# Kernel tuning notes

Hardware: AMD Instinct MI355X
Metric: run time of the kernel (lower is better)

The kernel has to match this reference:

```python
import jax, jax.numpy as jnp
import numpy as np

N = 100000      # nodes
E = 3200000     # edges (avg degree 32)
FEA = 67
HID = 16
OUT = 2
K = 3           # num_stacks
T = 2           # num_layers


def setup_inputs() -> dict:
    key = jax.random.key(0)
    ks = jax.random.split(key, 11)
    s = 0.1  # weight init scale
    return {
        "x": jax.random.normal(ks[0], (N, FEA), jnp.float32),
        "edge_index": jax.random.randint(ks[1], (2, E), 0, N, dtype=jnp.int32),
        "init_w1": jax.random.normal(ks[2], (K, FEA, HID), jnp.float32) * s,
        "w1": jax.random.normal(ks[3], (1, K, HID, HID), jnp.float32) * s,
        "root_w1": jax.random.normal(ks[4], (1, K, FEA, HID), jnp.float32) * s,
        "b1": jax.random.normal(ks[5], (1, K, 1, HID), jnp.float32) * s,
        "init_w2": jax.random.normal(ks[6], (K, HID, OUT), jnp.float32) * s,
        "w2": jax.random.normal(ks[7], (1, K, OUT, OUT), jnp.float32) * s,
        "root_w2": jax.random.normal(ks[8], (1, K, HID, OUT), jnp.float32) * s,
        "b2": jax.random.normal(ks[9], (1, K, 1, OUT), jnp.float32) * s,
    }


def gcn_norm(src, dst, n):
    # symmetric normalization of A WITHOUT self-loops (PyG ARMAConv behavior)
    deg = jax.ops.segment_sum(jnp.ones(src.shape[0], jnp.float32), dst, num_segments=n)
    dinv = jnp.where(deg > 0, jax.lax.rsqrt(jnp.maximum(deg, 1.0)), 0.0)
    return dinv[src] * dinv[dst]  # [E]


def arma_conv(x, src, dst, norm, init_w, w, root_w, bias, act, n):
    # x: [N, Fin]; shared_weights=True, num_layers=T, num_stacks=K
    out = jnp.einsum('nf,kfh->knh', x, init_w)           # t=0 transform
    root = jnp.einsum('nf,kfh->knh', x, root_w[0])       # root term (dropout=identity in eval)
    for t in range(T):
        if t > 0:
            out = jnp.einsum('knh,khp->knp', out, w[0])
        # propagate: out[i] = sum_{(j->i)} norm_e * out[j]
        m = (out[:, src, :] * norm[None, :, None]).transpose(1, 0, 2)  # [E,K,H]
        agg = jax.ops.segment_sum(m, dst, num_segments=n).transpose(1, 0, 2)  # [K,N,H]
        out = agg + root + bias[0]
        if act:
            out = jax.nn.relu(out)
    return out.mean(axis=0)  # average over stacks -> [N, H]


def reference(x, edge_index, init_w1, w1, root_w1, b1, init_w2, w2, root_w2, b2):
    src, dst = edge_index[0], edge_index[1]
    n = x.shape[0]
    norm = gcn_norm(src, dst, n)
    h = jax.nn.relu(arma_conv(x, src, dst, norm, init_w1, w1, root_w1, b1, True, n))
    o = arma_conv(h, src, dst, norm, init_w2, w2, root_w2, b2, False, n)
    return jax.nn.log_softmax(o, axis=1)
```

## Files before the change

kernel.cpp:

```cpp
#include <hip/hip_runtime.h>
#include <hip/hip_fp16.h>
#include <math.h>

#define NN 100000
#define NE 3200000
#define FEA 67
#define HID 16
#define OUTC 2
#define KS 3
#define KH 48
#define KO 6
#define PAD 64

#define PB 512
#define EPB 6250
#define BINW 512
#define NBINS 196
#define M1 (NBINS * PB)
#define NSCB 98

#define TBM 128
#define TNB ((NN + TBM - 1) / TBM)
#define XS_STRIDE 132
#define WT_STRIDE 68


__global__ void k_hist(const int* __restrict__ dst, int* __restrict__ hist) {
    __shared__ int h[NBINS];
    if (threadIdx.x < NBINS) h[threadIdx.x] = 0;
    __syncthreads();
    int base = blockIdx.x * EPB;
    for (int i = threadIdx.x; i < EPB; i += 256)
        atomicAdd(&h[dst[base + i] >> 9], 1);
    __syncthreads();
    if (threadIdx.x < NBINS) hist[threadIdx.x * PB + blockIdx.x] = h[threadIdx.x];
}


__global__ void k_partial(const int* __restrict__ in, int* __restrict__ partials, int n) {
    __shared__ int s[256];
    int base = blockIdx.x * 1024;
    int acc = 0;
    for (int i = threadIdx.x; i < 1024; i += 256) {
        int idx = base + i;
        if (idx < n) acc += in[idx];
    }
    s[threadIdx.x] = acc;
    __syncthreads();
    for (int off = 128; off > 0; off >>= 1) {
        if (threadIdx.x < off) s[threadIdx.x] += s[threadIdx.x + off];
        __syncthreads();
    }
    if (threadIdx.x == 0) partials[blockIdx.x] = s[0];
}

__global__ void k_downsweepF(const int* __restrict__ in, const int* __restrict__ partials,
                             int* __restrict__ out, int n) {
    __shared__ int ps[256];
    __shared__ int s[256];
    int t = threadIdx.x;
    ps[t] = (t < NSCB) ? partials[t] : 0;
    __syncthreads();
    for (int off = 1; off < 256; off <<= 1) {
        int v = (t >= off) ? ps[t - off] : 0;
        __syncthreads();
        ps[t] += v;
        __syncthreads();
    }
    int bbase = (blockIdx.x > 0) ? ps[blockIdx.x - 1] : 0;

    int base = blockIdx.x * 1024 + t * 4;
    int d0 = 0, d1 = 0, d2 = 0, d3 = 0;
    if (base + 0 < n) d0 = in[base + 0];
    if (base + 1 < n) d1 = in[base + 1];
    if (base + 2 < n) d2 = in[base + 2];
    if (base + 3 < n) d3 = in[base + 3];
    int ts = d0 + d1 + d2 + d3;
    s[t] = ts;
    __syncthreads();
    for (int off = 1; off < 256; off <<= 1) {
        int v = (t >= off) ? s[t - off] : 0;
        __syncthreads();
        s[t] += v;
        __syncthreads();
    }
    int excl = s[t] - ts + bbase;
    if (base + 0 < n) out[base + 0] = excl;
    if (base + 1 < n) out[base + 1] = excl + d0;
    if (base + 2 < n) out[base + 2] = excl + d0 + d1;
    if (base + 3 < n) out[base + 3] = excl + d0 + d1 + d2;
}


__global__ void k_pass2(const int* __restrict__ src, const int* __restrict__ dst,
                        const int* __restrict__ hist_scan, int* __restrict__ recs) {
    __shared__ int curs[NBINS];
    if (threadIdx.x < NBINS) curs[threadIdx.x] = hist_scan[threadIdx.x * PB + blockIdx.x];
    __syncthreads();
    int base = blockIdx.x * EPB;
    for (int i = threadIdx.x; i < EPB; i += 256) {
        int e = base + i;
        int s = src[e], d = dst[e];
        int pos = atomicAdd(&curs[d >> 9], 1);
        recs[pos] = s | ((d & 511) << 17);
    }
}


__global__ void k_degsort(const int* __restrict__ recs, const int* __restrict__ hist_scan,
                          int* __restrict__ deg, float* __restrict__ dinv,
                          int* __restrict__ row_start, int* __restrict__ csr) {
    __shared__ int cnt[BINW];
    __shared__ int scn[BINW];
    int bin = blockIdx.x, t = threadIdx.x;
    cnt[t] = 0;
    __syncthreads();
    int s0 = hist_scan[bin * PB];
    int s1 = (bin + 1 < NBINS) ? hist_scan[(bin + 1) * PB] : NE;
    for (int r = s0 + t; r < s1; r += BINW)
        atomicAdd(&cnt[((unsigned)recs[r]) >> 17], 1);
    __syncthreads();
    scn[t] = cnt[t];
    __syncthreads();
    for (int off = 1; off < BINW; off <<= 1) {
        int v = (t >= off) ? scn[t - off] : 0;
        __syncthreads();
        scn[t] += v;
        __syncthreads();
    }
    int node = bin * BINW + t;
    int rs = s0 + scn[t] - cnt[t];
    if (node < NN) {
        int c = cnt[t];
        deg[node]       = c;
        dinv[node]      = (c > 0) ? rsqrtf((float)c) : 0.f;
        row_start[node] = rs;
    }
    scn[t] = rs;
    __syncthreads();
    for (int r = s0 + t; r < s1; r += BINW) {
        int rec = recs[r];
        int pos = atomicAdd(&scn[((unsigned)rec) >> 17], 1);
        csr[pos] = rec & 0x1FFFF;
    }
}


__global__ void k_transform1(const float* __restrict__ x, const float* __restrict__ iw,
                             const float* __restrict__ rw, const float* __restrict__ b1,
                             const float* __restrict__ dinv,
                             __half* __restrict__ A, __half* __restrict__ Bpad,
                             float* __restrict__ R) {
    if (blockIdx.x == TNB) {
        int t = threadIdx.x;
        if (t < PAD) A[(size_t)NN * PAD + t] = __float2half(0.f);
        else if (t < 2 * PAD) Bpad[(size_t)NN * PAD + (t - PAD)] = __float2half(0.f);
        return;
    }
    __shared__ float xs[FEA * XS_STRIDE];
    __shared__ float wTs[96 * WT_STRIDE];
    __shared__ float bb[KH];
    int n0g = blockIdx.x * TBM;

    for (int idx = threadIdx.x; idx < 96 * FEA; idx += 256) {
        int j = idx / FEA, f = idx % FEA;
        float v;
        if (j < KH) v = iw[(j >> 4) * (FEA * HID) + f * HID + (j & 15)];
        else { int jr = j - KH; v = rw[(jr >> 4) * (FEA * HID) + f * HID + (jr & 15)]; }
        wTs[j * WT_STRIDE + f] = v;
    }
    if (threadIdx.x < KH) bb[threadIdx.x] = b1[threadIdx.x];
    for (int idx = threadIdx.x; idx < TBM * FEA; idx += 256) {
        int nl = idx / FEA, f = idx % FEA;
        int n = n0g + nl;
        xs[f * XS_STRIDE + nl] = (n < NN) ? x[(size_t)n * FEA + f] : 0.f;
    }
    __syncthreads();

    int tx = threadIdx.x & 31, ty = threadIdx.x >> 5;
    int nl0 = tx * 4;
    int j0  = ty * 12;
    float acc[4][12];
    #pragma unroll
    for (int p = 0; p < 12; ++p) {
        float init = (j0 >= KH) ? bb[j0 - KH + p] : 0.f;
        acc[0][p] = init; acc[1][p] = init; acc[2][p] = init; acc[3][p] = init;
    }

    #pragma unroll 4
    for (int fb = 0; fb < 16; ++fb) {
        int f0 = fb * 4;
        float4 xv0 = *(const float4*)&xs[(f0 + 0) * XS_STRIDE + nl0];
        float4 xv1 = *(const float4*)&xs[(f0 + 1) * XS_STRIDE + nl0];
        float4 xv2 = *(const float4*)&xs[(f0 + 2) * XS_STRIDE + nl0];
        float4 xv3 = *(const float4*)&xs[(f0 + 3) * XS_STRIDE + nl0];
        #pragma unroll
        for (int p = 0; p < 12; ++p) {
            float4 wv = *(const float4*)&wTs[(j0 + p) * WT_STRIDE + f0];
            acc[0][p] += xv0.x * wv.x + xv1.x * wv.y + xv2.x * wv.z + xv3.x * wv.w;
            acc[1][p] += xv0.y * wv.x + xv1.y * wv.y + xv2.y * wv.z + xv3.y * wv.w;
            acc[2][p] += xv0.z * wv.x + xv1.z * wv.y + xv2.z * wv.z + xv3.z * wv.w;
            acc[3][p] += xv0.w * wv.x + xv1.w * wv.y + xv2.w * wv.z + xv3.w * wv.w;
        }
    }
    #pragma unroll
    for (int f = 64; f < FEA; ++f) {
        float x0 = xs[f * XS_STRIDE + nl0 + 0];
        float x1 = xs[f * XS_STRIDE + nl0 + 1];
        float x2 = xs[f * XS_STRIDE + nl0 + 2];
        float x3 = xs[f * XS_STRIDE + nl0 + 3];
        #pragma unroll
        for (int p = 0; p < 12; ++p) {
            float wv = wTs[(j0 + p) * WT_STRIDE + f];
            acc[0][p] += x0 * wv; acc[1][p] += x1 * wv;
            acc[2][p] += x2 * wv; acc[3][p] += x3 * wv;
        }
    }

    if (j0 < KH) {
        #pragma unroll
        for (int nq = 0; nq < 4; ++nq) {
            int n = n0g + nl0 + nq;
            if (n < NN) {
                float dv = dinv[n];
                __half2* Ap = (__half2*)A + (size_t)n * (PAD / 2) + (j0 >> 1);
                #pragma unroll
                for (int p2 = 0; p2 < 6; ++p2)
                    Ap[p2] = __halves2half2(__float2half_rn(acc[nq][2 * p2] * dv),
                                            __float2half_rn(acc[nq][2 * p2 + 1] * dv));
            }
        }
    } else {
        int jr = j0 - KH;
        #pragma unroll
        for (int nq = 0; nq < 4; ++nq) {
            int n = n0g + nl0 + nq;
            if (n < NN) {
                float* Rp = &R[(size_t)n * KH + jr];
                *(float4*)(Rp + 0) = make_float4(acc[nq][0], acc[nq][1], acc[nq][2],  acc[nq][3]);
                *(float4*)(Rp + 4) = make_float4(acc[nq][4], acc[nq][5], acc[nq][6],  acc[nq][7]);
                *(float4*)(Rp + 8) = make_float4(acc[nq][8], acc[nq][9], acc[nq][10], acc[nq][11]);
            }
        }
    }
}


template <bool FUSEW>
__global__ void k_spmm48(const __half2* __restrict__ Asrc,
                         const float* __restrict__ R,
                         const int* __restrict__ row_start, const int* __restrict__ deg,
                         const float* __restrict__ dinv, const int* __restrict__ csr,
                         const float* __restrict__ w1, __half2* __restrict__ Bout) {
    __shared__ float w1s[FUSEW ? KS * HID * HID : 1];
    if (FUSEW) {
        for (int i = threadIdx.x; i < KS * HID * HID; i += 256) w1s[i] = w1[i];
        __syncthreads();
    }
    int node = (blockIdx.x * 256 + threadIdx.x) >> 6;
    int lane = threadIdx.x & 63;
    int eo   = lane >> 5;
    int cl   = lane & 31;
    int start = __builtin_amdgcn_readfirstlane(row_start[node]);
    int d     = __builtin_amdgcn_readfirstlane(deg[node]);
    float dv  = dinv[node];
    float ax = 0.f, ay = 0.f;
    for (int b = 0; b < d; b += 64) {
        int nb  = min(64, d - b);
        int myc = csr[start + b + lane];
        int npf = nb >> 1;
        int p = 0;
        for (; p + 4 <= npf; p += 4) {
            int c0 = __shfl(myc, 2 * (p + 0) + eo, 64);
            int c1 = __shfl(myc, 2 * (p + 1) + eo, 64);
            int c2 = __shfl(myc, 2 * (p + 2) + eo, 64);
            int c3 = __shfl(myc, 2 * (p + 3) + eo, 64);
            float2 f0 = __half22float2(Asrc[(size_t)c0 * (PAD / 2) + cl]);
            float2 f1 = __half22float2(Asrc[(size_t)c1 * (PAD / 2) + cl]);
            float2 f2 = __half22float2(Asrc[(size_t)c2 * (PAD / 2) + cl]);
            float2 f3 = __half22float2(Asrc[(size_t)c3 * (PAD / 2) + cl]);
            ax += f0.x + f1.x; ay += f0.y + f1.y;
            ax += f2.x + f3.x; ay += f2.y + f3.y;
        }
        for (; p < npf; ++p) {
            int c = __shfl(myc, 2 * p + eo, 64);
            float2 f = __half22float2(Asrc[(size_t)c * (PAD / 2) + cl]);
            ax += f.x; ay += f.y;
        }
        if (nb & 1) {
            int c = __shfl(myc, nb - 1, 64);
            c = (eo == 0) ? c : NN;
            float2 f = __half22float2(Asrc[(size_t)c * (PAD / 2) + cl]);
            ax += f.x; ay += f.y;
        }
    }
    ax += __shfl_xor(ax, 32, 64);
    ay += __shfl_xor(ay, 32, 64);
    float2 r2 = make_float2(0.f, 0.f);
    if (cl < 24) r2 = *(const float2*)&R[(size_t)node * KH + 2 * cl];
    float vx = fmaxf(ax * dv + r2.x, 0.f);
    float vy = fmaxf(ay * dv + r2.y, 0.f);
    if (FUSEW) {
        int k  = cl >> 3;
        int p0 = (2 * cl) & 15;
        float o0 = 0.f, o1 = 0.f;
        #pragma unroll
        for (int h2 = 0; h2 < 8; ++h2) {
            float ix = __shfl(vx, k * 8 + h2, 64);
            float iy = __shfl(vy, k * 8 + h2, 64);
            o0 += ix * w1s[k * 256 + (2 * h2) * 16 + p0]     + iy * w1s[k * 256 + (2 * h2 + 1) * 16 + p0];
            o1 += ix * w1s[k * 256 + (2 * h2) * 16 + p0 + 1] + iy * w1s[k * 256 + (2 * h2 + 1) * 16 + p0 + 1];
        }
        if (eo == 0 && cl < 24)
            Bout[(size_t)node * (PAD / 2) + cl] =
                __halves2half2(__float2half_rn(o0 * dv), __float2half_rn(o1 * dv));
    } else {
        if (eo == 0 && cl < 24)
            Bout[(size_t)node * (PAD / 2) + cl] =
                __halves2half2(__float2half_rn(vx), __float2half_rn(vy));
    }
}


__global__ void k_mt2(const __half* __restrict__ L1, const float* __restrict__ iw,
                      const float* __restrict__ rw, const float* __restrict__ b2,
                      const float* __restrict__ dinv,
                      float* __restrict__ A2, float* __restrict__ R2) {
    __shared__ float wi[KS * HID * OUTC];
    __shared__ float wr_[KS * HID * OUTC];
    __shared__ float bb[KO];
    if (threadIdx.x < KS * HID * OUTC) { wi[threadIdx.x] = iw[threadIdx.x]; wr_[threadIdx.x] = rw[threadIdx.x]; }
    if (threadIdx.x < KO) bb[threadIdx.x] = b2[threadIdx.x];
    __syncthreads();
    int n = blockIdx.x * 256 + threadIdx.x;
    if (n >= NN) return;
    const __half2* hp = (const __half2*)(L1 + (size_t)n * PAD);
    float v[KH];
    #pragma unroll
    for (int q = 0; q < 24; ++q) {
        float2 f = __half22float2(hp[q]);
        v[q * 2 + 0] = f.x; v[q * 2 + 1] = f.y;
    }
    float h[HID];
    #pragma unroll
    for (int hh = 0; hh < HID; ++hh)
        h[hh] = fmaxf((v[hh] + v[16 + hh] + v[32 + hh]) * (1.f / 3.f), 0.f);
    float dv = dinv[n];
    #pragma unroll
    for (int k = 0; k < KS; ++k) {
        #pragma unroll
        for (int o = 0; o < OUTC; ++o) {
            float a = 0.f, r = bb[k * 2 + o];
            #pragma unroll
            for (int hh = 0; hh < HID; ++hh) {
                a += h[hh] * wi[k * 32 + hh * 2 + o];
                r += h[hh] * wr_[k * 32 + hh * 2 + o];
            }
            A2[n * KO + k * 2 + o] = a * dv;
            R2[n * KO + k * 2 + o] = r;
        }
    }
}


__global__ void k_spmm6_g(const float* __restrict__ Asrc, const float* __restrict__ R2,
                          const int* __restrict__ row_start, const int* __restrict__ deg,
                          const float* __restrict__ dinv, const int* __restrict__ csr,
                          const float* __restrict__ w2, float* __restrict__ Bout) {
    __shared__ float ws[KS * OUTC * OUTC];
    if (threadIdx.x < KS * OUTC * OUTC) ws[threadIdx.x] = w2[threadIdx.x];
    __syncthreads();
    int t = blockIdx.x * 256 + threadIdx.x;
    int node = t / KO, j = t % KO;
    bool active = node < NN;
    float acc = 0.f, r = 0.f, dv = 0.f;
    int start = 0, d = 0;
    if (active) {
        start = row_start[node];
        d     = deg[node];
        r     = R2[node * KO + j];
        dv    = dinv[node];
    }
    int e = 0;
    for (; e + 4 <= d; e += 4) {
        int c0 = csr[start + e + 0];
        int c1 = csr[start + e + 1];
        int c2 = csr[start + e + 2];
        int c3 = csr[start + e + 3];
        acc += Asrc[c0 * KO + j];
        acc += Asrc[c1 * KO + j];
        acc += Asrc[c2 * KO + j];
        acc += Asrc[c3 * KO + j];
    }
    for (; e < d; ++e)
        acc += Asrc[csr[start + e] * KO + j];
    float v = acc * dv + r;
    float other = __shfl_xor(v, 1, 64);
    if (active) {
        int k = j >> 1, p = j & 1;
        float v0 = (p == 0) ? v : other;
        float v1 = (p == 0) ? other : v;
        Bout[node * KO + j] = (v0 * ws[k * 4 + p] + v1 * ws[k * 4 + 2 + p]) * dv;
    }
}


__global__ void k_spmm6_f(const float* __restrict__ Asrc, const float* __restrict__ R2,
                          const int* __restrict__ row_start, const int* __restrict__ deg,
                          const float* __restrict__ dinv, const int* __restrict__ csr,
                          float* __restrict__ out) {
    int wave = threadIdx.x >> 6;
    int l    = threadIdx.x & 63;
    int nl   = l / 6;
    int j    = l - nl * 6;
    bool active = nl < 10;
    int node = blockIdx.x * 40 + wave * 10 + nl;
    float acc = 0.f, r = 0.f, dv = 0.f;
    int start = 0, d = 0;
    if (active) {
        start = row_start[node];
        d     = deg[node];
        r     = R2[node * KO + j];
        dv    = dinv[node];
    }
    int e = 0;
    for (; e + 4 <= d; e += 4) {
        int c0 = csr[start + e + 0];
        int c1 = csr[start + e + 1];
        int c2 = csr[start + e + 2];
        int c3 = csr[start + e + 3];
        acc += Asrc[c0 * KO + j];
        acc += Asrc[c1 * KO + j];
        acc += Asrc[c2 * KO + j];
        acc += Asrc[c3 * KO + j];
    }
    for (; e < d; ++e)
        acc += Asrc[csr[start + e] * KO + j];
    float v = acc * dv + r;
    int base = nl * 6;
    float o0 = (__shfl(v, base + 0, 64) + __shfl(v, base + 2, 64) + __shfl(v, base + 4, 64)) * (1.f / 3.f);
    float o1 = (__shfl(v, base + 1, 64) + __shfl(v, base + 3, 64) + __shfl(v, base + 5, 64)) * (1.f / 3.f);
    if (active && j == 0) {
        float m = fmaxf(o0, o1);
        float ls = m + logf(expf(o0 - m) + expf(o1 - m));
        *(float2*)(out + (size_t)node * 2) = make_float2(o0 - ls, o1 - ls);
    }
}


extern "C" void kernel_launch(void* const* d_in, const int* in_sizes, int n_in,
                              void* d_out, int out_size, void* d_ws, size_t ws_size,
                              hipStream_t stream) {
    const float* x   = (const float*)d_in[0];
    const int*   ei  = (const int*)d_in[1];
    const float* iw1 = (const float*)d_in[2];
    const float* w1  = (const float*)d_in[3];
    const float* rw1 = (const float*)d_in[4];
    const float* b1  = (const float*)d_in[5];
    const float* iw2 = (const float*)d_in[6];
    const float* w2  = (const float*)d_in[7];
    const float* rw2 = (const float*)d_in[8];
    const float* b2  = (const float*)d_in[9];
    const int* src = ei;
    const int* dst = ei + NE;
    float* out = (float*)d_out;

    char* ws = (char*)d_ws;
    size_t o = 0;
    int*    deg       = (int*)(ws + o);    o += (size_t)NN * 4;
    int*    row_start = (int*)(ws + o);    o += (size_t)NN * 4;
    float*  dinv      = (float*)(ws + o);  o += (size_t)NN * 4;
    int*    hist      = (int*)(ws + o);    o += (size_t)M1 * 4;
    int*    hist_scan = (int*)(ws + o);    o += (size_t)M1 * 4;
    int*    partials  = (int*)(ws + o);    o += 128 * 4;
    int*    csr       = (int*)(ws + o);    o += (size_t)(NE + 64) * 4;
    __half* A         = (__half*)(ws + o); o += (size_t)(NN + 1) * PAD * 2;
    float*  R         = (float*)(ws + o);  o += (size_t)NN * KH * 4;
    __half* B         = (__half*)(ws + o); o += (size_t)(NN + 1) * PAD * 2;
    int*    recs  = (int*)A;
    __half* L1f   = A;
    float*  A2    = R;
    float*  R2    = R + (size_t)NN * KO;
    float*  C2    = R + (size_t)NN * KO * 2;

    k_hist       <<<PB, 256, 0, stream>>>(dst, hist);
    k_partial    <<<NSCB, 256, 0, stream>>>(hist, partials, M1);
    k_downsweepF <<<NSCB, 256, 0, stream>>>(hist, partials, hist_scan, M1);
    k_pass2      <<<PB, 256, 0, stream>>>(src, dst, hist_scan, recs);
    k_degsort    <<<NBINS, BINW, 0, stream>>>(recs, hist_scan, deg, dinv, row_start, csr);

    k_transform1    <<<TNB + 1, 256, 0, stream>>>(x, iw1, rw1, b1, dinv, A, B, R);
    k_spmm48<true>  <<<NN / 4, 256, 0, stream>>>((const __half2*)A, R, row_start, deg, dinv, csr, w1, (__half2*)B);
    k_spmm48<false> <<<NN / 4, 256, 0, stream>>>((const __half2*)B, R, row_start, deg, dinv, csr, w1, (__half2*)L1f);

    k_mt2      <<<(NN + 255) / 256, 256, 0, stream>>>(L1f, iw2, rw2, b2, dinv, A2, R2);
    k_spmm6_g  <<<(NN * KO + 255) / 256, 256, 0, stream>>>(A2, R2, row_start, deg, dinv, csr, w2, C2);
    k_spmm6_f  <<<NN / 40, 256, 0, stream>>>(C2, R2, row_start, deg, dinv, csr, out);
}
```

Before: 330.8 us.

## Pad CSR rows to multiples of four and gather 8-byte chunks in SpMM48

The CSR build now pads each node's adjacency row to a multiple of four with dummy index NN, which points at a zero row, and offsets each bin so the padding fits. The 48-channel SpMM is restructured so four groups of 16 lanes each handle one edge per step, loading 8 bytes per lane instead of a half2. Because rows are padded, the odd-degree tail handling goes away, and the fused weight matmul and the stores use float4/uint2 vectors. The cost is extra padded gathers of the zero row, a wider reduction, and possible misalignment for the other SpMM kernels that read the padded csr with the original deg.

```diff
diff --git a/kernel.cpp b/kernel.cpp
--- a/kernel.cpp
+++ b/kernel.cpp
@@ -18,6 +18,7 @@
 #define NBINS 196
 #define M1 (NBINS * PB)
 #define NSCB 98
+#define CSR_CAP (NE + NBINS * 3 * BINW + 64)
 
 #define TBM 128
 #define TNB ((NN + TBM - 1) / TBM)
@@ -120,7 +121,9 @@
     for (int r = s0 + t; r < s1; r += BINW)
         atomicAdd(&cnt[((unsigned)recs[r]) >> 17], 1);
     __syncthreads();
-    scn[t] = cnt[t];
+    int c  = cnt[t];
+    int c4 = (c + 3) & ~3;
+    scn[t] = c4;
     __syncthreads();
     for (int off = 1; off < BINW; off <<= 1) {
         int v = (t >= off) ? scn[t - off] : 0;
@@ -128,10 +131,10 @@
         scn[t] += v;
         __syncthreads();
     }
+    int base = s0 + bin * (3 * BINW);
+    int rs   = base + scn[t] - c4;
     int node = bin * BINW + t;
-    int rs = s0 + scn[t] - cnt[t];
     if (node < NN) {
-        int c = cnt[t];
         deg[node]       = c;
         dinv[node]      = (c > 0) ? rsqrtf((float)c) : 0.f;
         row_start[node] = rs;
@@ -143,6 +146,9 @@
         int pos = atomicAdd(&scn[((unsigned)rec) >> 17], 1);
         csr[pos] = rec & 0x1FFFF;
     }
+    __syncthreads();
+    int e4 = rs + c4;
+    for (int i = scn[t]; i < e4; ++i) csr[i] = NN;
 }
 
 
@@ -247,11 +253,11 @@
 
 
 template <bool FUSEW>
-__global__ void k_spmm48(const __half2* __restrict__ Asrc,
+__global__ void k_spmm48(const __half* __restrict__ Asrc,
                          const float* __restrict__ R,
                          const int* __restrict__ row_start, const int* __restrict__ deg,
                          const float* __restrict__ dinv, const int* __restrict__ csr,
-                         const float* __restrict__ w1, __half2* __restrict__ Bout) {
+                         const float* __restrict__ w1, __half* __restrict__ Bout) {
     __shared__ float w1s[FUSEW ? KS * HID * HID : 1];
     if (FUSEW) {
         for (int i = threadIdx.x; i < KS * HID * HID; i += 256) w1s[i] = w1[i];
@@ -259,65 +265,71 @@
     }
     int node = (blockIdx.x * 256 + threadIdx.x) >> 6;
     int lane = threadIdx.x & 63;
-    int eo   = lane >> 5;
-    int cl   = lane & 31;
+    int g    = lane >> 4;
+    int q    = lane & 15;
     int start = __builtin_amdgcn_readfirstlane(row_start[node]);
     int d     = __builtin_amdgcn_readfirstlane(deg[node]);
-    float dv  = dinv[node];
-    float ax = 0.f, ay = 0.f;
-    for (int b = 0; b < d; b += 64) {
-        int nb  = min(64, d - b);
+    int d4    = (d + 3) & ~3;
+    float4 acc = make_float4(0.f, 0.f, 0.f, 0.f);
+    unsigned qoff = (unsigned)(q << 3);
+    for (int b = 0; b < d4; b += 64) {
+        int nb  = min(64, d4 - b);
         int myc = csr[start + b + lane];
-        int npf = nb >> 1;
-        int p = 0;
-        for (; p + 4 <= npf; p += 4) {
-            int c0 = __shfl(myc, 2 * (p + 0) + eo, 64);
-            int c1 = __shfl(myc, 2 * (p + 1) + eo, 64);
-            int c2 = __shfl(myc, 2 * (p + 2) + eo, 64);
-            int c3 = __shfl(myc, 2 * (p + 3) + eo, 64);
-            float2 f0 = __half22float2(Asrc[(size_t)c0 * (PAD / 2) + cl]);
-            float2 f1 = __half22float2(Asrc[(size_t)c1 * (PAD / 2) + cl]);
-            float2 f2 = __half22float2(Asrc[(size_t)c2 * (PAD / 2) + cl]);
-            float2 f3 = __half22float2(Asrc[(size_t)c3 * (PAD / 2) + cl]);
-            ax += f0.x + f1.x; ay += f0.y + f1.y;
-            ax += f2.x + f3.x; ay += f2.y + f3.y;
-        }
-        for (; p < npf; ++p) {
-            int c = __shfl(myc, 2 * p + eo, 64);
-            float2 f = __half22float2(Asrc[(size_t)c * (PAD / 2) + cl]);
-            ax += f.x; ay += f.y;
-        }
-        if (nb & 1) {
-            int c = __shfl(myc, nb - 1, 64);
-            c = (eo == 0) ? c : NN;
-            float2 f = __half22float2(Asrc[(size_t)c * (PAD / 2) + cl]);
-            ax += f.x; ay += f.y;
-        }
-    }
-    ax += __shfl_xor(ax, 32, 64);
-    ay += __shfl_xor(ay, 32, 64);
-    float2 r2 = make_float2(0.f, 0.f);
-    if (cl < 24) r2 = *(const float2*)&R[(size_t)node * KH + 2 * cl];
-    float vx = fmaxf(ax * dv + r2.x, 0.f);
-    float vy = fmaxf(ay * dv + r2.y, 0.f);
+        #pragma unroll 4
+        for (int p = 0; p < nb; p += 4) {
+            int c = __shfl(myc, p + g, 64);
+            uint2 hv = *(const uint2*)((const char*)Asrc + (((unsigned)c << 7) + qoff));
+            float2 f0 = __half22float2(*(__half2*)&hv.x);
+            float2 f1 = __half22float2(*(__half2*)&hv.y);
+            acc.x += f0.x; acc.y += f0.y; acc.z += f1.x; acc.w += f1.y;
+        }
+    }
+    acc.x += __shfl_xor(acc.x, 16, 64); acc.y += __shfl_xor(acc.y, 16, 64);
+    acc.z += __shfl_xor(acc.z, 16, 64); acc.w += __shfl_xor(acc.w, 16, 64);
+    acc.x += __shfl_xor(acc.x, 32, 64); acc.y += __shfl_xor(acc.y, 32, 64);
+    acc.z += __shfl_xor(acc.z, 32, 64); acc.w += __shfl_xor(acc.w, 32, 64);
+
+    float dv = dinv[node];
+    float4 r4 = make_float4(0.f, 0.f, 0.f, 0.f);
+    if (q < 12) r4 = *(const float4*)&R[(size_t)node * KH + (q << 2)];
+    float4 v;
+    v.x = fmaxf(acc.x * dv + r4.x, 0.f);
+    v.y = fmaxf(acc.y * dv + r4.y, 0.f);
+    v.z = fmaxf(acc.z * dv + r4.z, 0.f);
+    v.w = fmaxf(acc.w * dv + r4.w, 0.f);
+
+    float4 o;
     if (FUSEW) {
-        int k  = cl >> 3;
-        int p0 = (2 * cl) & 15;
-        float o0 = 0.f, o1 = 0.f;
+        int kk = q >> 2; if (kk > 2) kk = 2;
+        int p0 = (q & 3) << 2;
+        o = make_float4(0.f, 0.f, 0.f, 0.f);
         #pragma unroll
-        for (int h2 = 0; h2 < 8; ++h2) {
-            float ix = __shfl(vx, k * 8 + h2, 64);
-            float iy = __shfl(vy, k * 8 + h2, 64);
-            o0 += ix * w1s[k * 256 + (2 * h2) * 16 + p0]     + iy * w1s[k * 256 + (2 * h2 + 1) * 16 + p0];
-            o1 += ix * w1s[k * 256 + (2 * h2) * 16 + p0 + 1] + iy * w1s[k * 256 + (2 * h2 + 1) * 16 + p0 + 1];
-        }
-        if (eo == 0 && cl < 24)
-            Bout[(size_t)node * (PAD / 2) + cl] =
-                __halves2half2(__float2half_rn(o0 * dv), __float2half_rn(o1 * dv));
+        for (int hq = 0; hq < 4; ++hq) {
+            int srcl = kk * 4 + hq;
+            float i0 = __shfl(v.x, srcl, 64);
+            float i1 = __shfl(v.y, srcl, 64);
+            float i2 = __shfl(v.z, srcl, 64);
+            float i3 = __shfl(v.w, srcl, 64);
+            const float* wrow = &w1s[kk * 256 + (4 * hq) * 16 + p0];
+            float4 w0 = *(const float4*)(wrow);
+            float4 w1v = *(const float4*)(wrow + 16);
+            float4 w2v = *(const float4*)(wrow + 32);
+            float4 w3v = *(const float4*)(wrow + 48);
+            o.x += i0 * w0.x + i1 * w1v.x + i2 * w2v.x + i3 * w3v.x;
+            o.y += i0 * w0.y + i1 * w1v.y + i2 * w2v.y + i3 * w3v.y;
+            o.z += i0 * w0.z + i1 * w1v.z + i2 * w2v.z + i3 * w3v.z;
+            o.w += i0 * w0.w + i1 * w1v.w + i2 * w2v.w + i3 * w3v.w;
+        }
+        o.x *= dv; o.y *= dv; o.z *= dv; o.w *= dv;
     } else {
-        if (eo == 0 && cl < 24)
-            Bout[(size_t)node * (PAD / 2) + cl] =
-                __halves2half2(__float2half_rn(vx), __float2half_rn(vy));
+        o = v;
+    }
+    if (lane < 12) {
+        __half2 lo = __halves2half2(__float2half_rn(o.x), __float2half_rn(o.y));
+        __half2 hi = __halves2half2(__float2half_rn(o.z), __float2half_rn(o.w));
+        uint2 u;
+        u.x = *(unsigned*)&lo; u.y = *(unsigned*)&hi;
+        *(uint2*)((char*)Bout + ((size_t)node << 7) + (lane << 3)) = u;
     }
 }
 
@@ -473,7 +485,7 @@
     int*    hist      = (int*)(ws + o);    o += (size_t)M1 * 4;
     int*    hist_scan = (int*)(ws + o);    o += (size_t)M1 * 4;
     int*    partials  = (int*)(ws + o);    o += 128 * 4;
-    int*    csr       = (int*)(ws + o);    o += (size_t)(NE + 64) * 4;
+    int*    csr       = (int*)(ws + o);    o += (size_t)CSR_CAP * 4;
     __half* A         = (__half*)(ws + o); o += (size_t)(NN + 1) * PAD * 2;
     float*  R         = (float*)(ws + o);  o += (size_t)NN * KH * 4;
     __half* B         = (__half*)(ws + o); o += (size_t)(NN + 1) * PAD * 2;
@@ -490,8 +502,8 @@
     k_degsort    <<<NBINS, BINW, 0, stream>>>(recs, hist_scan, deg, dinv, row_start, csr);
 
     k_transform1    <<<TNB + 1, 256, 0, stream>>>(x, iw1, rw1, b1, dinv, A, B, R);
-    k_spmm48<true>  <<<NN / 4, 256, 0, stream>>>((const __half2*)A, R, row_start, deg, dinv, csr, w1, (__half2*)B);
-    k_spmm48<false> <<<NN / 4, 256, 0, stream>>>((const __half2*)B, R, row_start, deg, dinv, csr, w1, (__half2*)L1f);
+    k_spmm48<true>  <<<NN / 4, 256, 0, stream>>>(A, R, row_start, deg, dinv, csr, w1, B);
+    k_spmm48<false> <<<NN / 4, 256, 0, stream>>>(B, R, row_start, deg, dinv, csr, w1, L1f);
 
     k_mt2      <<<(NN + 255) / 256, 256, 0, stream>>>(L1f, iw2, rw2, b2, dinv, A2, R2);
     k_spmm6_g  <<<(NN * KO + 255) / 256, 256, 0, stream>>>(A2, R2, row_start, deg, dinv, csr, w2, C2);
```

Result: slower. 352.3 us (+6.5%).

## Pad CSR rows to multiples of four and accumulate SpMM in half2

Applied to the files above, without the earlier changes.

Each node's CSR row is padded to a multiple of four entries, with the padding filled by the dummy zero node index, so the SpMM inner loop drops its remainder and odd-tail branches and becomes one uniform unrolled loop. Accumulation switches from fp32 to packed half2 adds, halving the conversion and add work per gathered element. Column indices are read with nontemporal loads. This trades extra CSR storage and wasted gathers of the zero row against simpler control flow, and fp16 accumulation over about 32 neighbours risks precision loss.

```diff
diff --git a/kernel.cpp b/kernel.cpp
--- a/kernel.cpp
+++ b/kernel.cpp
@@ -18,6 +18,7 @@
 #define NBINS 196
 #define M1 (NBINS * PB)
 #define NSCB 98
+#define CSR_CAP (NE + NBINS * 3 * BINW + 64)
 
 #define TBM 128
 #define TNB ((NN + TBM - 1) / TBM)
@@ -120,7 +121,9 @@
     for (int r = s0 + t; r < s1; r += BINW)
         atomicAdd(&cnt[((unsigned)recs[r]) >> 17], 1);
     __syncthreads();
-    scn[t] = cnt[t];
+    int c  = cnt[t];
+    int c4 = (c + 3) & ~3;
+    scn[t] = c4;
     __syncthreads();
     for (int off = 1; off < BINW; off <<= 1) {
         int v = (t >= off) ? scn[t - off] : 0;
@@ -128,10 +131,10 @@
         scn[t] += v;
         __syncthreads();
     }
+    int base = s0 + bin * (3 * BINW);
+    int rs   = base + scn[t] - c4;
     int node = bin * BINW + t;
-    int rs = s0 + scn[t] - cnt[t];
     if (node < NN) {
-        int c = cnt[t];
         deg[node]       = c;
         dinv[node]      = (c > 0) ? rsqrtf((float)c) : 0.f;
         row_start[node] = rs;
@@ -143,6 +146,9 @@
         int pos = atomicAdd(&scn[((unsigned)rec) >> 17], 1);
         csr[pos] = rec & 0x1FFFF;
     }
+    __syncthreads();
+    int e4 = rs + c4;
+    for (int i = scn[t]; i < e4; ++i) csr[i] = NN;
 }
 
 
@@ -263,43 +269,30 @@
     int cl   = lane & 31;
     int start = __builtin_amdgcn_readfirstlane(row_start[node]);
     int d     = __builtin_amdgcn_readfirstlane(deg[node]);
+    int d4    = (d + 3) & ~3;
     float dv  = dinv[node];
-    float ax = 0.f, ay = 0.f;
-    for (int b = 0; b < d; b += 64) {
-        int nb  = min(64, d - b);
-        int myc = csr[start + b + lane];
-        int npf = nb >> 1;
-        int p = 0;
-        for (; p + 4 <= npf; p += 4) {
-            int c0 = __shfl(myc, 2 * (p + 0) + eo, 64);
-            int c1 = __shfl(myc, 2 * (p + 1) + eo, 64);
-            int c2 = __shfl(myc, 2 * (p + 2) + eo, 64);
-            int c3 = __shfl(myc, 2 * (p + 3) + eo, 64);
-            float2 f0 = __half22float2(Asrc[(size_t)c0 * (PAD / 2) + cl]);
-            float2 f1 = __half22float2(Asrc[(size_t)c1 * (PAD / 2) + cl]);
-            float2 f2 = __half22float2(Asrc[(size_t)c2 * (PAD / 2) + cl]);
-            float2 f3 = __half22float2(Asrc[(size_t)c3 * (PAD / 2) + cl]);
-            ax += f0.x + f1.x; ay += f0.y + f1.y;
-            ax += f2.x + f3.x; ay += f2.y + f3.y;
-        }
-        for (; p < npf; ++p) {
-            int c = __shfl(myc, 2 * p + eo, 64);
-            float2 f = __half22float2(Asrc[(size_t)c * (PAD / 2) + cl]);
-            ax += f.x; ay += f.y;
-        }
-        if (nb & 1) {
-            int c = __shfl(myc, nb - 1, 64);
-            c = (eo == 0) ? c : NN;
-            float2 f = __half22float2(Asrc[(size_t)c * (PAD / 2) + cl]);
-            ax += f.x; ay += f.y;
-        }
-    }
-    ax += __shfl_xor(ax, 32, 64);
-    ay += __shfl_xor(ay, 32, 64);
     float2 r2 = make_float2(0.f, 0.f);
     if (cl < 24) r2 = *(const float2*)&R[(size_t)node * KH + 2 * cl];
-    float vx = fmaxf(ax * dv + r2.x, 0.f);
-    float vy = fmaxf(ay * dv + r2.y, 0.f);
+
+    __half2 hacc = __halves2half2(__float2half(0.f), __float2half(0.f));
+    for (int b = 0; b < d4; b += 64) {
+        int nb  = min(64, d4 - b);
+        int myc = __builtin_nontemporal_load(&csr[start + b + lane]);
+        int npf = nb >> 1;
+        #pragma unroll 4
+        for (int p = 0; p < npf; ++p) {
+            int c = __shfl(myc, 2 * p + eo, 64);
+            __half2 hv = Asrc[(size_t)c * (PAD / 2) + cl];
+            hacc = __hadd2(hacc, hv);
+        }
+    }
+    unsigned u  = *(unsigned*)&hacc;
+    unsigned uo = __shfl_xor((int)u, 32, 64);
+    hacc = __hadd2(hacc, *(__half2*)&uo);
+    float2 f = __half22float2(hacc);
+    float vx = fmaxf(f.x * dv + r2.x, 0.f);
+    float vy = fmaxf(f.y * dv + r2.y, 0.f);
+
     if (FUSEW) {
         int k  = cl >> 3;
         int p0 = (2 * cl) & 15;
@@ -473,7 +466,7 @@
     int*    hist      = (int*)(ws + o);    o += (size_t)M1 * 4;
     int*    hist_scan = (int*)(ws + o);    o += (size_t)M1 * 4;
     int*    partials  = (int*)(ws + o);    o += 128 * 4;
-    int*    csr       = (int*)(ws + o);    o += (size_t)(NE + 64) * 4;
+    int*    csr       = (int*)(ws + o);    o += (size_t)CSR_CAP * 4;
     __half* A         = (__half*)(ws + o); o += (size_t)(NN + 1) * PAD * 2;
     float*  R         = (float*)(ws + o);  o += (size_t)NN * KH * 4;
     __half* B         = (__half*)(ws + o); o += (size_t)(NN + 1) * PAD * 2;
```

After: 418.5 us. 26.5% more time.

## Pad CSR rows to multiple of four and store root term in fp16

Applied to the files above, without the earlier changes.

CSR rows are padded to a multiple of four entries, with the extra slots pointing at the zero sentinel node. This lets the spmm48 loop drop its odd-tail branch and run only full unrolled iterations. The root/residual term R moves from fp32 to fp16, halving its footprint and read traffic, and its load is hoisted before the gather loop. The cost is extra sentinel gathers, a larger CSR buffer, and reduced precision in the root term; other kernels that read the CSR (spmm6) now see the padded row starts.

```diff
diff --git a/kernel.cpp b/kernel.cpp
--- a/kernel.cpp
+++ b/kernel.cpp
@@ -18,6 +18,7 @@
 #define NBINS 196
 #define M1 (NBINS * PB)
 #define NSCB 98
+#define CSR_CAP (NE + NBINS * 3 * BINW + 64)
 
 #define TBM 128
 #define TNB ((NN + TBM - 1) / TBM)
@@ -120,7 +121,9 @@
     for (int r = s0 + t; r < s1; r += BINW)
         atomicAdd(&cnt[((unsigned)recs[r]) >> 17], 1);
     __syncthreads();
-    scn[t] = cnt[t];
+    int c  = cnt[t];
+    int c4 = (c + 3) & ~3;
+    scn[t] = c4;
     __syncthreads();
     for (int off = 1; off < BINW; off <<= 1) {
         int v = (t >= off) ? scn[t - off] : 0;
@@ -128,10 +131,10 @@
         scn[t] += v;
         __syncthreads();
     }
+    int base = s0 + bin * (3 * BINW);
+    int rs   = base + scn[t] - c4;
     int node = bin * BINW + t;
-    int rs = s0 + scn[t] - cnt[t];
     if (node < NN) {
-        int c = cnt[t];
         deg[node]       = c;
         dinv[node]      = (c > 0) ? rsqrtf((float)c) : 0.f;
         row_start[node] = rs;
@@ -143,6 +146,9 @@
         int pos = atomicAdd(&scn[((unsigned)rec) >> 17], 1);
         csr[pos] = rec & 0x1FFFF;
     }
+    __syncthreads();
+    int e4 = rs + c4;
+    for (int i = scn[t]; i < e4; ++i) csr[i] = NN;
 }
 
 
@@ -150,7 +156,7 @@
                              const float* __restrict__ rw, const float* __restrict__ b1,
                              const float* __restrict__ dinv,
                              __half* __restrict__ A, __half* __restrict__ Bpad,
-                             float* __restrict__ R) {
+                             __half2* __restrict__ Rh) {
     if (blockIdx.x == TNB) {
         int t = threadIdx.x;
         if (t < PAD) A[(size_t)NN * PAD + t] = __float2half(0.f);
@@ -231,15 +237,16 @@
             }
         }
     } else {
-        int jr = j0 - KH;
+        int jh = (j0 - KH) >> 1;
         #pragma unroll
         for (int nq = 0; nq < 4; ++nq) {
             int n = n0g + nl0 + nq;
             if (n < NN) {
-                float* Rp = &R[(size_t)n * KH + jr];
-                *(float4*)(Rp + 0) = make_float4(acc[nq][0], acc[nq][1], acc[nq][2],  acc[nq][3]);
-                *(float4*)(Rp + 4) = make_float4(acc[nq][4], acc[nq][5], acc[nq][6],  acc[nq][7]);
-                *(float4*)(Rp + 8) = make_float4(acc[nq][8], acc[nq][9], acc[nq][10], acc[nq][11]);
+                __half2* Rp = Rh + (size_t)n * 24 + jh;
+                #pragma unroll
+                for (int p2 = 0; p2 < 6; ++p2)
+                    Rp[p2] = __halves2half2(__float2half_rn(acc[nq][2 * p2]),
+                                            __float2half_rn(acc[nq][2 * p2 + 1]));
             }
         }
     }
@@ -248,7 +255,7 @@
 
 template <bool FUSEW>
 __global__ void k_spmm48(const __half2* __restrict__ Asrc,
-                         const float* __restrict__ R,
+                         const __half2* __restrict__ Rh,
                          const int* __restrict__ row_start, const int* __restrict__ deg,
                          const float* __restrict__ dinv, const int* __restrict__ csr,
                          const float* __restrict__ w1, __half2* __restrict__ Bout) {
@@ -263,10 +270,14 @@
     int cl   = lane & 31;
     int start = __builtin_amdgcn_readfirstlane(row_start[node]);
     int d     = __builtin_amdgcn_readfirstlane(deg[node]);
+    int d4    = (d + 3) & ~3;
     float dv  = dinv[node];
+    float2 r2 = make_float2(0.f, 0.f);
+    if (cl < 24) r2 = __half22float2(Rh[(size_t)node * 24 + cl]);
+
     float ax = 0.f, ay = 0.f;
-    for (int b = 0; b < d; b += 64) {
-        int nb  = min(64, d - b);
+    for (int b = 0; b < d4; b += 64) {
+        int nb  = min(64, d4 - b);
         int myc = csr[start + b + lane];
         int npf = nb >> 1;
         int p = 0;
@@ -287,19 +298,12 @@
             float2 f = __half22float2(Asrc[(size_t)c * (PAD / 2) + cl]);
             ax += f.x; ay += f.y;
         }
-        if (nb & 1) {
-            int c = __shfl(myc, nb - 1, 64);
-            c = (eo == 0) ? c : NN;
-            float2 f = __half22float2(Asrc[(size_t)c * (PAD / 2) + cl]);
-            ax += f.x; ay += f.y;
-        }
     }
     ax += __shfl_xor(ax, 32, 64);
     ay += __shfl_xor(ay, 32, 64);
-    float2 r2 = make_float2(0.f, 0.f);
-    if (cl < 24) r2 = *(const float2*)&R[(size_t)node * KH + 2 * cl];
     float vx = fmaxf(ax * dv + r2.x, 0.f);
     float vy = fmaxf(ay * dv + r2.y, 0.f);
+
     if (FUSEW) {
         int k  = cl >> 3;
         int p0 = (2 * cl) & 15;
@@ -467,21 +471,21 @@
 
     char* ws = (char*)d_ws;
     size_t o = 0;
-    int*    deg       = (int*)(ws + o);    o += (size_t)NN * 4;
-    int*    row_start = (int*)(ws + o);    o += (size_t)NN * 4;
-    float*  dinv      = (float*)(ws + o);  o += (size_t)NN * 4;
-    int*    hist      = (int*)(ws + o);    o += (size_t)M1 * 4;
-    int*    hist_scan = (int*)(ws + o);    o += (size_t)M1 * 4;
-    int*    partials  = (int*)(ws + o);    o += 128 * 4;
-    int*    csr       = (int*)(ws + o);    o += (size_t)(NE + 64) * 4;
-    __half* A         = (__half*)(ws + o); o += (size_t)(NN + 1) * PAD * 2;
-    float*  R         = (float*)(ws + o);  o += (size_t)NN * KH * 4;
-    __half* B         = (__half*)(ws + o); o += (size_t)(NN + 1) * PAD * 2;
+    int*     deg       = (int*)(ws + o);     o += (size_t)NN * 4;
+    int*     row_start = (int*)(ws + o);     o += (size_t)NN * 4;
+    float*   dinv      = (float*)(ws + o);   o += (size_t)NN * 4;
+    int*     hist      = (int*)(ws + o);     o += (size_t)M1 * 4;
+    int*     hist_scan = (int*)(ws + o);     o += (size_t)M1 * 4;
+    int*     partials  = (int*)(ws + o);     o += 128 * 4;
+    int*     csr       = (int*)(ws + o);     o += (size_t)CSR_CAP * 4;
+    __half*  A         = (__half*)(ws + o);  o += (size_t)(NN + 1) * PAD * 2;
+    __half2* Rh        = (__half2*)(ws + o); o += (size_t)NN * 24 * 4;
+    __half*  B         = (__half*)(ws + o);  o += (size_t)(NN + 1) * PAD * 2;
     int*    recs  = (int*)A;
     __half* L1f   = A;
-    float*  A2    = R;
-    float*  R2    = R + (size_t)NN * KO;
-    float*  C2    = R + (size_t)NN * KO * 2;
+    float*  A2    = (float*)Rh;
+    float*  R2    = (float*)Rh + (size_t)NN * KO;
+    float*  C2    = (float*)Rh + (size_t)NN * KO * 2;
 
     k_hist       <<<PB, 256, 0, stream>>>(dst, hist);
     k_partial    <<<NSCB, 256, 0, stream>>>(hist, partials, M1);
@@ -489,9 +493,9 @@
     k_pass2      <<<PB, 256, 0, stream>>>(src, dst, hist_scan, recs);
     k_degsort    <<<NBINS, BINW, 0, stream>>>(recs, hist_scan, deg, dinv, row_start, csr);
 
-    k_transform1    <<<TNB + 1, 256, 0, stream>>>(x, iw1, rw1, b1, dinv, A, B, R);
-    k_spmm48<true>  <<<NN / 4, 256, 0, stream>>>((const __half2*)A, R, row_start, deg, dinv, csr, w1, (__half2*)B);
-    k_spmm48<false> <<<NN / 4, 256, 0, stream>>>((const __half2*)B, R, row_start, deg, dinv, csr, w1, (__half2*)L1f);
+    k_transform1    <<<TNB + 1, 256, 0, stream>>>(x, iw1, rw1, b1, dinv, A, B, Rh);
+    k_spmm48<true>  <<<NN / 4, 256, 0, stream>>>((const __half2*)A, Rh, row_start, deg, dinv, csr, w1, (__half2*)B);
+    k_spmm48<false> <<<NN / 4, 256, 0, stream>>>((const __half2*)B, Rh, row_start, deg, dinv, csr, w1, (__half2*)L1f);
 
     k_mt2      <<<(NN + 255) / 256, 256, 0, stream>>>(L1f, iw2, rw2, b2, dinv, A2, R2);
     k_spmm6_g  <<<(NN * KO + 255) / 256, 256, 0, stream>>>(A2, R2, row_start, deg, dinv, csr, w2, C2);
```

After: 324.0 us. 2.1% less time.
